# Optimization experiments

Measured on AMD Instinct MI355X. Metric: run time of the kernel, lower is better.

Reference implementation:

```python
import jax, jax.numpy as jnp
import numpy as np

B, N, D_IN, D, H, L, NQ, NC, HID = 4, 25000, 32, 256, 8, 6, 100, 18, 1024


def _ln(x, g, b, eps=1e-5):
    m = jnp.mean(x, -1, keepdims=True)
    v = jnp.mean((x - m) ** 2, -1, keepdims=True)
    return (x - m) / jnp.sqrt(v + eps) * g + b


def _mha(q, kv, wqkv, bqkv, wo, bo, h):
    # q: (B, Lq, d), kv: (B, Lk, d); torch nn.MultiheadAttention math
    d = q.shape[-1]
    dh = d // h
    wq, wk, wv = jnp.split(wqkv, 3, axis=0)
    bq, bk, bv = jnp.split(bqkv, 3)
    Q = (q @ wq.T + bq).reshape(q.shape[0], q.shape[1], h, dh)
    K = (kv @ wk.T + bk).reshape(kv.shape[0], kv.shape[1], h, dh)
    V = (kv @ wv.T + bv).reshape(kv.shape[0], kv.shape[1], h, dh)
    s = jnp.einsum('bqhd,bkhd->bhqk', Q, K) / jnp.asarray(np.sqrt(dh), Q.dtype)
    a = jax.nn.softmax(s, axis=-1)
    o = jnp.einsum('bhqk,bkhd->bqhd', a, V).reshape(q.shape)
    return o @ wo.T + bo


def setup_inputs() -> dict:
    key = jax.random.key(0)
    ks = list(jax.random.split(key, 20))
    ki = iter(ks)

    def p(shape, s=0.02):
        return jax.random.normal(next(ki), shape, jnp.float32) * s

    inp = {
        'x': jax.random.normal(next(ki), (B * N, D_IN), jnp.float32),
        'batch_offsets': jnp.arange(B + 1, dtype=jnp.int32) * N,
        'ip_w': p((D, D_IN)), 'ip_b': jnp.zeros((D,), jnp.float32),
        'ip_ln_g': jnp.ones((D,), jnp.float32), 'ip_ln_b': jnp.zeros((D,), jnp.float32),
        'xm_w1': p((D, D_IN)), 'xm_b1': jnp.zeros((D,), jnp.float32),
        'xm_w2': p((D, D)), 'xm_b2': jnp.zeros((D,), jnp.float32),
        'query_embed': p((NQ, D), 1.0),
        'ca_wqkv': p((L, 3 * D, D)), 'ca_bqkv': jnp.zeros((L, 3 * D), jnp.float32),
        'ca_wo': p((L, D, D)), 'ca_bo': jnp.zeros((L, D), jnp.float32),
        'sa_wqkv': p((L, 3 * D, D)), 'sa_bqkv': jnp.zeros((L, 3 * D), jnp.float32),
        'sa_wo': p((L, D, D)), 'sa_bo': jnp.zeros((L, D), jnp.float32),
        'sa_ln_g': jnp.ones((L, D), jnp.float32), 'sa_ln_b': jnp.zeros((L, D), jnp.float32),
        'ffn_w1': p((L, HID, D)), 'ffn_b1': jnp.zeros((L, HID), jnp.float32),
        'ffn_w2': p((L, D, HID)), 'ffn_b2': jnp.zeros((L, D), jnp.float32),
        'ffn_ln_g': jnp.ones((L, D), jnp.float32), 'ffn_ln_b': jnp.zeros((L, D), jnp.float32),
        'out_ln_g': jnp.ones((D,), jnp.float32), 'out_ln_b': jnp.zeros((D,), jnp.float32),
        'cls_w1': p((D, D)), 'cls_b1': jnp.zeros((D,), jnp.float32),
        'cls_w2': p((NC + 1, D)), 'cls_b2': jnp.zeros((NC + 1,), jnp.float32),
    }
    return inp


def reference(x, batch_offsets, ip_w, ip_b, ip_ln_g, ip_ln_b, xm_w1, xm_b1, xm_w2, xm_b2,
              query_embed, ca_wqkv, ca_bqkv, ca_wo, ca_bo, sa_wqkv, sa_bqkv, sa_wo, sa_bo,
              sa_ln_g, sa_ln_b, ffn_w1, ffn_b1, ffn_w2, ffn_b2, ffn_ln_g, ffn_ln_b,
              out_ln_g, out_ln_b, cls_w1, cls_b1, cls_w2, cls_b2):
    b = batch_offsets.shape[0] - 1  # uniform segments -> batched attention
    n = x.shape[0] // b
    # input_proj: Linear -> LayerNorm -> ReLU
    inst = jax.nn.relu(_ln(x @ ip_w.T + ip_b, ip_ln_g, ip_ln_b)).reshape(b, n, -1)
    # x_mask: Linear -> ReLU -> Linear
    mask_feats = (jax.nn.relu(x @ xm_w1.T + xm_b1) @ xm_w2.T + xm_b2).reshape(b, n, -1)
    query = jnp.broadcast_to(query_embed, (b,) + query_embed.shape)
    for i in range(ca_wqkv.shape[0]):
        # CrossAttentionLayer: NOTE original discards dropout/norm results -> pure residual
        query = _mha(query, inst, ca_wqkv[i], ca_bqkv[i], ca_wo[i], ca_bo[i], H) + query
        # SelfAttentionLayer: residual + LayerNorm
        query = _ln(_mha(query, query, sa_wqkv[i], sa_bqkv[i], sa_wo[i], sa_bo[i], H) + query,
                    sa_ln_g[i], sa_ln_b[i])
        # FFN: residual + LayerNorm
        ff = jax.nn.relu(query @ ffn_w1[i].T + ffn_b1[i]) @ ffn_w2[i].T + ffn_b2[i]
        query = _ln(ff + query, ffn_ln_g[i], ffn_ln_b[i])
    qn = _ln(query, out_ln_g, out_ln_b)
    pred_labels = jax.nn.relu(qn @ cls_w1.T + cls_b1) @ cls_w2.T + cls_b2  # (b, NQ, NC+1)
    pred_masks = jnp.einsum('bqd,bnd->bqn', qn, mask_feats)  # (b, NQ, n)
    return pred_labels, pred_masks
```

## Files before the change

kernel.cpp:

```cpp
#include <hip/hip_runtime.h>

typedef unsigned short u16;
typedef unsigned int   u32;

constexpr int Bz   = 4;
constexpr int Ni   = 25000;
constexpr int BNi  = Bz * Ni;
constexpr int DIN  = 32;
constexpr int D    = 256;
constexpr int Hh   = 8;
constexpr int DH   = 32;
constexpr int Ll   = 6;
constexpr int NQ   = 100;
constexpr int NC1  = 19;
constexpr int HIDd = 1024;

constexpr int CHUNK  = 1250;
constexpr int NCHUNK = Ni / CHUNK;
constexpr size_t PARTB = (size_t)Hh * NCHUNK * 128 * 34;
constexpr float SM_SCALE = 0.17677669529663687f;

__device__ __forceinline__ u16 f2b(float f) {
    union { __bf16 h; u16 u; } c; c.h = (__bf16)f; return c.u;
}
__device__ __forceinline__ u32 pk2(float a, float b) {
    union { __bf16 h[2]; u32 u; } c; c.h[0] = (__bf16)a; c.h[1] = (__bf16)b; return c.u;
}

__global__ void k_cvt(const float* __restrict__ in, u16* __restrict__ out, int n) {
    for (int i = blockIdx.x * blockDim.x + threadIdx.x; i < n; i += gridDim.x * blockDim.x)
        out[i] = f2b(in[i]);
}

struct CvtJobs { const float* s[9]; u16* d[9]; int n[9]; };
__global__ __launch_bounds__(256) void k_cvtall(CvtJobs j) {
    const int job = blockIdx.y;
    const float* s = j.s[job];
    u16* d = j.d[job];
    const int n = j.n[job];
    for (int i = blockIdx.x * 256 + threadIdx.x; i < n; i += gridDim.x * 256)
        d[i] = f2b(s[i]);
}

__device__ __forceinline__ void gload16(const u16* g, u16* l) {
    __builtin_amdgcn_global_load_lds(
        (const __attribute__((address_space(1))) void*)g,
        (__attribute__((address_space(3))) void*)l, 16, 0, 0);
}

typedef __attribute__((ext_vector_type(8))) __bf16 bf8v;
typedef __attribute__((ext_vector_type(8))) short  s8v;
typedef __attribute__((ext_vector_type(4))) float  f4v;

template<bool DOLN>
__global__ __launch_bounds__(512) void k_inproj(
    const float* __restrict__ x, int row0, int Mloc,
    const u16* __restrict__ w16, const float* __restrict__ bias,
    const float* __restrict__ g, const float* __restrict__ bb,
    u16* __restrict__ outb)
{
    __shared__ u16 Ws[256 * 40];
    __shared__ float Cb[256], Cg[256], Cbb[256];
    const int tid = threadIdx.x, lane = tid & 63, w = tid >> 6;
    const int lr = lane & 15, hi = lane >> 4;

    for (int ch = tid; ch < 1024; ch += 512) {
        int r = ch >> 2, g4 = ch & 3;
        *(uint4*)&Ws[r * 40 + g4 * 8] = *(const uint4*)(w16 + r * 32 + g4 * 8);
    }
    if (tid < 256) {
        Cb[tid] = bias[tid];
        if (DOLN) { Cg[tid] = g[tid]; Cbb[tid] = bb[tid]; }
    }

    const int rloc = blockIdx.x * 128 + w * 16 + lr;
    const int gr = row0 + min(rloc, Mloc - 1);
    bf8v xf;
    {
        const float* xp = x + (size_t)gr * DIN + hi * 8;
        float4 a = *(const float4*)xp, c = *(const float4*)(xp + 4);
        union { s8v s; bf8v b; } u;
        u.s[0] = (short)f2b(a.x); u.s[1] = (short)f2b(a.y);
        u.s[2] = (short)f2b(a.z); u.s[3] = (short)f2b(a.w);
        u.s[4] = (short)f2b(c.x); u.s[5] = (short)f2b(c.y);
        u.s[6] = (short)f2b(c.z); u.s[7] = (short)f2b(c.w);
        xf = u.b;
    }
    __syncthreads();

    f4v acc[16];
    #pragma unroll
    for (int ci = 0; ci < 16; ci++) {
        acc[ci] = (f4v){0.f, 0.f, 0.f, 0.f};
        bf8v af = *(const bf8v*)&Ws[(ci * 16 + lr) * 40 + hi * 8];
        acc[ci] = __builtin_amdgcn_mfma_f32_16x16x32_bf16(af, xf, acc[ci], 0, 0, 0);
    }
    #pragma unroll
    for (int ci = 0; ci < 16; ci++)
        #pragma unroll
        for (int r = 0; r < 4; r++)
            acc[ci][r] += Cb[ci * 16 + hi * 4 + r];

    float mean = 0.f, ri = 1.f;
    if (DOLN) {
        float s = 0.f, q = 0.f;
        #pragma unroll
        for (int ci = 0; ci < 16; ci++)
            #pragma unroll
            for (int r = 0; r < 4; r++) { s += acc[ci][r]; q += acc[ci][r] * acc[ci][r]; }
        s += __shfl_xor(s, 16); s += __shfl_xor(s, 32);
        q += __shfl_xor(q, 16); q += __shfl_xor(q, 32);
        mean = s * (1.f / D);
        float var = q * (1.f / D) - mean * mean;
        ri = rsqrtf(var + 1e-5f);
    }
    if (rloc < Mloc) {
        #pragma unroll
        for (int ci = 0; ci < 16; ci++) {
            float v0[4];
            #pragma unroll
            for (int r = 0; r < 4; r++) {
                float v = acc[ci][r];
                if (DOLN) v = (v - mean) * ri * Cg[ci * 16 + hi * 4 + r] + Cbb[ci * 16 + hi * 4 + r];
                v0[r] = fmaxf(v, 0.f);
            }
            uint2 pkv;
            pkv.x = pk2(v0[0], v0[1]);
            pkv.y = pk2(v0[2], v0[3]);
            *(uint2*)&outb[(size_t)rloc * 256 + ci * 16 + hi * 4] = pkv;
        }
    }
}

__global__ __launch_bounds__(256) void k_ln(
    const float* __restrict__ in, float* __restrict__ out,
    const float* __restrict__ g, const float* __restrict__ b)
{
    const int t = threadIdx.x;
    const int row = blockIdx.x;
    float v = in[(size_t)row * D + t];
    float s = v, q = v * v;
    #pragma unroll
    for (int off = 32; off >= 1; off >>= 1) { s += __shfl_xor(s, off); q += __shfl_xor(q, off); }
    __shared__ float red[2][4];
    const int wid = t >> 6;
    if ((t & 63) == 0) { red[0][wid] = s; red[1][wid] = q; }
    __syncthreads();
    float S = red[0][0] + red[0][1] + red[0][2] + red[0][3];
    float Q = red[1][0] + red[1][1] + red[1][2] + red[1][3];
    float m   = S * (1.f / D);
    float var = Q * (1.f / D) - m * m;
    float ri  = rsqrtf(var + 1e-5f);
    out[(size_t)row * D + t] = (v - m) * ri * g[t] + b[t];
}

__global__ __launch_bounds__(256) void k_bcast(const float* __restrict__ qe, float* __restrict__ q)
{
    const int t = threadIdx.x;
    const int r = blockIdx.x;
    q[(size_t)r * D + t] = qe[(size_t)(r % NQ) * D + t];
}

template<int BM, int BN, int TM, int TN>
__global__ __launch_bounds__(256) void k_gemm(
    const float* __restrict__ A, const float* __restrict__ W,
    const float* __restrict__ bias, const float* __restrict__ resid,
    float* __restrict__ C, int M, int N, int K, int relu)
{
    constexpr int BK = 16;
    constexpr int TX = BN / TN, TY = BM / TM;
    static_assert(TX * TY == 256, "block must be 256 threads");
    __shared__ float As[BK][BM + 4];
    __shared__ float Ws[BK][BN + 4];

    const int tid = threadIdx.x;
    const int tx = tid % TX, ty = tid / TX;
    const int row0 = blockIdx.y * BM, col0 = blockIdx.x * BN;

    float acc[TM][TN];
    #pragma unroll
    for (int i = 0; i < TM; i++)
        #pragma unroll
        for (int j = 0; j < TN; j++) acc[i][j] = 0.f;

    for (int k0 = 0; k0 < K; k0 += BK) {
        __syncthreads();
        for (int idx = tid; idx < BM * (BK / 4); idx += 256) {
            int r = idx / (BK / 4), c4 = idx % (BK / 4);
            int gr = row0 + r;
            float4 v;
            if (gr < M) v = *(const float4*)(A + (size_t)gr * K + k0 + c4 * 4);
            else { v.x = v.y = v.z = v.w = 0.f; }
            As[c4*4+0][r] = v.x; As[c4*4+1][r] = v.y; As[c4*4+2][r] = v.z; As[c4*4+3][r] = v.w;
        }
        for (int idx = tid; idx < BN * (BK / 4); idx += 256) {
            int n = idx / (BK / 4), c4 = idx % (BK / 4);
            int gn = col0 + n;
            float4 v;
            if (gn < N) v = *(const float4*)(W + (size_t)gn * K + k0 + c4 * 4);
            else { v.x = v.y = v.z = v.w = 0.f; }
            Ws[c4*4+0][n] = v.x; Ws[c4*4+1][n] = v.y; Ws[c4*4+2][n] = v.z; Ws[c4*4+3][n] = v.w;
        }
        __syncthreads();
        #pragma unroll
        for (int kk = 0; kk < BK; kk++) {
            float a[TM], bb[TN];
            #pragma unroll
            for (int i = 0; i < TM; i++) a[i] = As[kk][ty * TM + i];
            #pragma unroll
            for (int j = 0; j < TN; j++) bb[j] = Ws[kk][tx * TN + j];
            #pragma unroll
            for (int i = 0; i < TM; i++)
                #pragma unroll
                for (int j = 0; j < TN; j++)
                    acc[i][j] = fmaf(a[i], bb[j], acc[i][j]);
        }
    }

    #pragma unroll
    for (int i = 0; i < TM; i++) {
        int gr = row0 + ty * TM + i;
        if (gr >= M) continue;
        #pragma unroll
        for (int j = 0; j < TN; j++) {
            int gn = col0 + tx * TN + j;
            if (gn >= N) continue;
            float v = acc[i][j];
            if (bias)  v += bias[gn];
            if (resid) v += resid[(size_t)gr * N + gn];
            if (relu)  v = fmaxf(v, 0.f);
            C[(size_t)gr * N + gn] = v;
        }
    }
}

template<bool RELU>
__global__ __launch_bounds__(256) void mm_small(
    const float* __restrict__ A, const u16* __restrict__ W,
    const float* __restrict__ bias, const float* __restrict__ resid,
    float* __restrict__ C, int M, int N, int K)
{
    __shared__ u16 As[64 * 40];
    __shared__ u16 Bs[64 * 40];
    const int tid  = threadIdx.x;
    const int lane = tid & 63, w = tid >> 6;
    const int wm = w >> 1, wn = w & 1;
    const int row0 = blockIdx.y * 64, col0 = blockIdx.x * 64;
    const int lr = lane & 15, hi = lane >> 4;

    f4v acc[2][2];
    #pragma unroll
    for (int i = 0; i < 2; i++)
        #pragma unroll
        for (int j = 0; j < 2; j++) acc[i][j] = (f4v){0.f, 0.f, 0.f, 0.f};

    const int sr = tid >> 2, sc = (tid & 3) * 8;
    const float* ap = A + (size_t)min(row0 + sr, M - 1) * K + sc;
    const u16*   wpp = W + (size_t)min(col0 + sr, N - 1) * K + sc;
    u16* lA = &As[sr * 40 + sc];
    u16* lB = &Bs[sr * 40 + sc];

    for (int k0 = 0; k0 < K; k0 += 32) {
        __syncthreads();
        {
            float4 a = *(const float4*)ap, c = *(const float4*)(ap + 4);
            uint4 u;
            u.x = pk2(a.x, a.y); u.y = pk2(a.z, a.w);
            u.z = pk2(c.x, c.y); u.w = pk2(c.z, c.w);
            *(uint4*)lA = u;
            *(uint4*)lB = *(const uint4*)wpp;
            ap += 32; wpp += 32;
        }
        __syncthreads();
        bf8v a0 = *(const bf8v*)&As[(wm * 32      + lr) * 40 + hi * 8];
        bf8v a1 = *(const bf8v*)&As[(wm * 32 + 16 + lr) * 40 + hi * 8];
        bf8v b0 = *(const bf8v*)&Bs[(wn * 32      + lr) * 40 + hi * 8];
        bf8v b1 = *(const bf8v*)&Bs[(wn * 32 + 16 + lr) * 40 + hi * 8];
        acc[0][0] = __builtin_amdgcn_mfma_f32_16x16x32_bf16(a0, b0, acc[0][0], 0, 0, 0);
        acc[0][1] = __builtin_amdgcn_mfma_f32_16x16x32_bf16(a0, b1, acc[0][1], 0, 0, 0);
        acc[1][0] = __builtin_amdgcn_mfma_f32_16x16x32_bf16(a1, b0, acc[1][0], 0, 0, 0);
        acc[1][1] = __builtin_amdgcn_mfma_f32_16x16x32_bf16(a1, b1, acc[1][1], 0, 0, 0);
    }

    const int crl = hi * 4, ccl = lr;
    #pragma unroll
    for (int mi = 0; mi < 2; mi++)
        #pragma unroll
        for (int ni = 0; ni < 2; ni++)
            #pragma unroll
            for (int r = 0; r < 4; r++) {
                int grow = row0 + wm * 32 + mi * 16 + crl + r;
                int gcol = col0 + wn * 32 + ni * 16 + ccl;
                if (grow < M && gcol < N) {
                    float v = acc[mi][ni][r];
                    if (bias)  v += bias[gcol];
                    if (resid) v += resid[(size_t)grow * N + gcol];
                    if (RELU)  v = fmaxf(v, 0.f);
                    C[(size_t)grow * N + gcol] = v;
                }
            }
}

template<bool OUTBF>
__global__ __launch_bounds__(256) void mm128(
    const u16* __restrict__ A, const u16* __restrict__ W,
    const float* __restrict__ bias, void* __restrict__ Cv,
    int M, int N, int K, long long sA, long long sW, long long sC,
    int zmod, long long sW2, long long sBias)
{
    __shared__ u16 sm[8192];
    u16* As = sm;
    u16* Bs = sm + 4096;

    const int gx = gridDim.x, gy = gridDim.y;
    const int total = gx * gy * (int)gridDim.z;
    const int flat = blockIdx.x + gx * (blockIdx.y + gy * blockIdx.z);
    const int q8 = total >> 3, r8 = total & 7;
    const int xcd = flat & 7, blk = flat >> 3;
    const int swz = (xcd < r8 ? xcd * (q8 + 1) : r8 * (q8 + 1) + (xcd - r8) * q8) + blk;
    const int bx = swz % gx, by = (swz / gx) % gy, bz = swz / (gx * gy);

    const int aidx = bz % zmod, widx = bz / zmod;
    A += (size_t)aidx * sA;
    W += (size_t)aidx * sW + (size_t)widx * sW2;
    if (bias) bias += (size_t)widx * sBias;
    const int tid = threadIdx.x, lane = tid & 63, w = tid >> 6;
    const int wm = w >> 1, wn = w & 1;
    const int row0 = by * 128, col0 = bx * 128;
    const int lr = lane & 15, hi = lane >> 4;
    const int srow = lane >> 2, scol = (lane & 3) * 8;

    f4v acc[4][4];
    #pragma unroll
    for (int i = 0; i < 4; i++)
        #pragma unroll
        for (int j = 0; j < 4; j++) acc[i][j] = (f4v){0.f, 0.f, 0.f, 0.f};

    const int c0 = w * 2, c1 = w * 2 + 1;
    const u16* pa0 = A + (size_t)min(row0 + c0 * 16 + srow, M - 1) * K + scol;
    const u16* pa1 = A + (size_t)min(row0 + c1 * 16 + srow, M - 1) * K + scol;
    const u16* pb0 = W + (size_t)min(col0 + c0 * 16 + srow, N - 1) * K + scol;
    const u16* pb1 = W + (size_t)min(col0 + c1 * 16 + srow, N - 1) * K + scol;
    u16* la0 = &As[c0 * 512];
    u16* la1 = &As[c1 * 512];
    u16* lb0 = &Bs[c0 * 512];
    u16* lb1 = &Bs[c1 * 512];

    for (int k0 = 0; k0 < K; k0 += 32) {
        __syncthreads();
        gload16(pa0, la0); gload16(pa1, la1);
        gload16(pb0, lb0); gload16(pb1, lb1);
        pa0 += 32; pa1 += 32; pb0 += 32; pb1 += 32;
        __syncthreads();
        bf8v a[4], bb[4];
        #pragma unroll
        for (int mi = 0; mi < 4; mi++)
            a[mi] = *(const bf8v*)&As[(wm * 64 + mi * 16 + lr) * 32 + hi * 8];
        #pragma unroll
        for (int ni = 0; ni < 4; ni++)
            bb[ni] = *(const bf8v*)&Bs[(wn * 64 + ni * 16 + lr) * 32 + hi * 8];
        #pragma unroll
        for (int mi = 0; mi < 4; mi++)
            #pragma unroll
            for (int ni = 0; ni < 4; ni++)
                acc[mi][ni] = __builtin_amdgcn_mfma_f32_16x16x32_bf16(a[mi], bb[ni], acc[mi][ni], 0, 0, 0);
    }

    if (OUTBF) {
        #pragma unroll
        for (int h0 = 0; h0 < 2; h0++) {
            __syncthreads();
            if (wm == h0) {
                #pragma unroll
                for (int mi = 0; mi < 4; mi++)
                    #pragma unroll
                    for (int ni = 0; ni < 4; ni++) {
                        int gcol = col0 + wn * 64 + ni * 16 + lr;
                        float bv = bias ? bias[gcol] : 0.f;
                        #pragma unroll
                        for (int r = 0; r < 4; r++) {
                            int lrow = mi * 16 + hi * 4 + r;
                            sm[lrow * 128 + wn * 64 + ni * 16 + lr] = f2b(acc[mi][ni][r] + bv);
                        }
                    }
            }
            __syncthreads();
            u16* Cb16 = (u16*)Cv + (size_t)bz * sC;
            #pragma unroll
            for (int j = 0; j < 4; j++) {
                int idx = tid + j * 256;
                int lrow = idx >> 4, c16 = idx & 15;
                int grow = row0 + h0 * 64 + lrow;
                if (grow < M)
                    *(uint4*)(Cb16 + (size_t)grow * N + col0 + c16 * 8) =
                        *(const uint4*)&sm[lrow * 128 + c16 * 8];
            }
        }
    } else {
        const int crl = hi * 4, ccl = lr;
        float* Cf = (float*)Cv + (size_t)bz * sC;
        #pragma unroll
        for (int mi = 0; mi < 4; mi++)
            #pragma unroll
            for (int ni = 0; ni < 4; ni++)
                #pragma unroll
                for (int r = 0; r < 4; r++) {
                    int grow = row0 + wm * 64 + mi * 16 + crl + r;
                    int gcol = col0 + wn * 64 + ni * 16 + ccl;
                    if (grow < M && gcol < N) {
                        float v = acc[mi][ni][r];
                        if (bias) v += bias[gcol];
                        Cf[(size_t)grow * N + gcol] = v;
                    }
                }
    }
}

__global__ __launch_bounds__(512) void k_flash(
    const float* __restrict__ qbuf, const u16* __restrict__ kv,
    float* __restrict__ part, int bBase, size_t kvStride, size_t pStride)
{
    const int tid = threadIdx.x;
    const int lane = tid & 63, w = tid >> 6;
    const int h = blockIdx.y;
    const int b = bBase + blockIdx.z;
    const u16* kvp = kv + (size_t)blockIdx.z * kvStride;
    float* pp = part + (size_t)blockIdx.z * pStride;
    const int k0loc = blockIdx.x * CHUNK;
    const int lr = lane & 15, hi = lane >> 4;

    __shared__ u16 Ks[64 * 40];
    __shared__ u16 Vt[32 * 72];
    __shared__ u16 Pt[8][16 * 72];

    const int qt = w * 16 + lr;
    const int qg = b * NQ + min(qt, NQ - 1);
    bf8v qf;
    {
        const float* Qp = qbuf + (size_t)qg * D + h * DH + hi * 8;
        union { s8v s; bf8v b; } qu;
        #pragma unroll
        for (int j = 0; j < 8; j++) qu.s[j] = (short)f2b(Qp[j] * SM_SCALE);
        qf = qu.b;
    }

    const int keyK = (tid < 256) ? (tid >> 2) : ((tid - 256) >> 2);
    const int gK = (tid < 256) ? (tid & 3) : ((tid - 256) & 3);
    const u16* kvbase = kvp + h * DH + gK * 8 + (tid < 256 ? 0 : D);

    float m = -1e30f, l = 0.f;
    f4v o0 = (f4v){0.f,0.f,0.f,0.f}, o1 = (f4v){0.f,0.f,0.f,0.f};

    constexpr int NSTEP = (CHUNK + 63) / 64;
    for (int s = 0; s < NSTEP; s++) {
        const int ck = k0loc + s * 64;
        const int nv = min(64, k0loc + CHUNK - ck);
        __syncthreads();
        {
            int krow = min(ck + keyK, Ni - 1);
            if (tid < 256) {
                *(uint4*)&Ks[keyK * 40 + gK * 8] =
                    *(const uint4*)(kvbase + (size_t)krow * (2 * D));
            } else {
                uint4 u = *(const uint4*)(kvbase + (size_t)krow * (2 * D));
                const u16* pu = (const u16*)&u;
                #pragma unroll
                for (int j = 0; j < 8; j++) Vt[(gK * 8 + j) * 72 + keyK] = pu[j];
            }
        }
        __syncthreads();

        f4v sf[4];
        #pragma unroll
        for (int j = 0; j < 4; j++) {
            bf8v kf = *(const bf8v*)&Ks[(j * 16 + lr) * 40 + hi * 8];
            sf[j] = (f4v){0.f,0.f,0.f,0.f};
            sf[j] = __builtin_amdgcn_mfma_f32_16x16x32_bf16(kf, qf, sf[j], 0, 0, 0);
        }

        float sv[16];
        #pragma unroll
        for (int j = 0; j < 4; j++)
            #pragma unroll
            for (int r = 0; r < 4; r++) {
                int key0 = j * 16 + hi * 4 + r;
                sv[j * 4 + r] = (key0 < nv) ? sf[j][r] : -1e30f;
            }
        float smax = sv[0];
        #pragma unroll
        for (int j = 1; j < 16; j++) smax = fmaxf(smax, sv[j]);
        smax = fmaxf(smax, __shfl_xor(smax, 16));
        smax = fmaxf(smax, __shfl_xor(smax, 32));
        float mnew  = fmaxf(m, smax);
        float scale = __expf(m - mnew);
        m = mnew;

        float pv[16];
        float psum = 0.f;
        #pragma unroll
        for (int j = 0; j < 16; j++) {
            pv[j] = __expf(sv[j] - mnew);
            psum += pv[j];
        }
        psum += __shfl_xor(psum, 16);
        psum += __shfl_xor(psum, 32);
        l = l * scale + psum;

        u16* pw = &Pt[w][lr * 72];
        #pragma unroll
        for (int j = 0; j < 4; j++) {
            *(u32*)&pw[j * 16 + hi * 4]     = pk2(pv[j*4+0], pv[j*4+1]);
            *(u32*)&pw[j * 16 + hi * 4 + 2] = pk2(pv[j*4+2], pv[j*4+3]);
        }

        const int qb4 = hi * 4;
        float f0 = __shfl(scale, qb4 + 0);
        float f1 = __shfl(scale, qb4 + 1);
        float f2 = __shfl(scale, qb4 + 2);
        float f3 = __shfl(scale, qb4 + 3);
        o0[0] *= f0; o0[1] *= f1; o0[2] *= f2; o0[3] *= f3;
        o1[0] *= f0; o1[1] *= f1; o1[2] *= f2; o1[3] *= f3;

        #pragma unroll
        for (int j = 0; j < 2; j++) {
            bf8v pf  = *(const bf8v*)&Pt[w][lr * 72 + j * 32 + hi * 8];
            bf8v vf0 = *(const bf8v*)&Vt[lr * 72 + j * 32 + hi * 8];
            bf8v vf1 = *(const bf8v*)&Vt[(16 + lr) * 72 + j * 32 + hi * 8];
            o0 = __builtin_amdgcn_mfma_f32_16x16x32_bf16(pf, vf0, o0, 0, 0, 0);
            o1 = __builtin_amdgcn_mfma_f32_16x16x32_bf16(pf, vf1, o1, 0, 0, 0);
        }
    }

    const size_t pbase = ((size_t)(h * NCHUNK + blockIdx.x) * 128) * 34;
    #pragma unroll
    for (int r = 0; r < 4; r++) {
        int qtr = w * 16 + hi * 4 + r;
        pp[pbase + (size_t)qtr * 34 + 2 + lr]      = o0[r];
        pp[pbase + (size_t)qtr * 34 + 2 + 16 + lr] = o1[r];
    }
    if (lane < 16) {
        pp[pbase + (size_t)(w * 16 + lane) * 34 + 0] = m;
        pp[pbase + (size_t)(w * 16 + lane) * 34 + 1] = l;
    }
}

__global__ __launch_bounds__(64) void k_fmerge(const float* __restrict__ part,
                                               float* __restrict__ abuf, int bBase, size_t pStride)
{
    const float* pz = part + (size_t)blockIdx.y * pStride;
    const int b = bBase + blockIdx.y;
    const int t = threadIdx.x;
    const int hq = blockIdx.x;
    const int h = hq / NQ, q = hq % NQ;
    float mmax = -1e30f;
    for (int c = 0; c < NCHUNK; c++)
        mmax = fmaxf(mmax, pz[((size_t)(h * NCHUNK + c) * 128 + q) * 34]);
    float L = 0.f, a = 0.f;
    for (int c = 0; c < NCHUNK; c++) {
        const float* p = &pz[((size_t)(h * NCHUNK + c) * 128 + q) * 34];
        float wv = __expf(p[0] - mmax);
        L += wv * p[1];
        if (t < DH) a += wv * p[2 + t];
    }
    if (t < DH)
        abuf[((size_t)(b * NQ + q)) * D + h * DH + t] = a / L;
}

__global__ __launch_bounds__(128) void k_sattn(const float* __restrict__ sqkv, float* __restrict__ abuf)
{
    const int tid = threadIdx.x;
    const int bh = blockIdx.x;
    const int b = bh >> 3, h = bh & 7;
    __shared__ float Ks[NQ][DH], Vs[NQ][DH];
    for (int idx = tid; idx < NQ * 8; idx += 128) {
        int kk = idx >> 3, f4 = idx & 7;
        const float* base = sqkv + ((size_t)(b * NQ + kk)) * (3 * D) + h * DH;
        *(float4*)&Ks[kk][f4 * 4] = *(const float4*)(base + D + f4 * 4);
        *(float4*)&Vs[kk][f4 * 4] = *(const float4*)(base + 2 * D + f4 * 4);
    }
    float qr[DH];
    const int q = tid;
    if (q < NQ) {
        const float* Qp = sqkv + ((size_t)(b * NQ + q)) * (3 * D) + h * DH;
        #pragma unroll
        for (int d = 0; d < DH; d += 4) {
            float4 v = *(const float4*)(Qp + d);
            qr[d] = v.x * SM_SCALE; qr[d+1] = v.y * SM_SCALE;
            qr[d+2] = v.z * SM_SCALE; qr[d+3] = v.w * SM_SCALE;
        }
    } else {
        #pragma unroll
        for (int d = 0; d < DH; d++) qr[d] = 0.f;
    }
    __syncthreads();
    float m = -1e30f, l = 0.f, acc[DH];
    #pragma unroll
    for (int d = 0; d < DH; d++) acc[d] = 0.f;
    for (int kk = 0; kk < NQ; kk++) {
        float sc = 0.f;
        #pragma unroll
        for (int d = 0; d < DH; d++) sc += qr[d] * Ks[kk][d];
        if (sc > m) {
            float r = __expf(m - sc);
            l *= r;
            #pragma unroll
            for (int d = 0; d < DH; d++) acc[d] *= r;
            m = sc;
        }
        float p = __expf(sc - m);
        l += p;
        #pragma unroll
        for (int d = 0; d < DH; d++) acc[d] += p * Vs[kk][d];
    }
    if (q < NQ) {
        float li = 1.f / l;
        float* o = abuf + ((size_t)(b * NQ + q)) * D + h * DH;
        #pragma unroll
        for (int d = 0; d < DH; d++) o[d] = acc[d] * li;
    }
}

extern "C" void kernel_launch(void* const* d_in, const int* in_sizes, int n_in,
                              void* d_out, int out_size, void* d_ws, size_t ws_size,
                              hipStream_t stream)
{
    const float* x        = (const float*)d_in[0];
    const float* ip_w     = (const float*)d_in[2];
    const float* ip_b     = (const float*)d_in[3];
    const float* ip_g     = (const float*)d_in[4];
    const float* ip_bb    = (const float*)d_in[5];
    const float* xm_w1    = (const float*)d_in[6];
    const float* xm_b1    = (const float*)d_in[7];
    const float* xm_w2    = (const float*)d_in[8];
    const float* xm_b2    = (const float*)d_in[9];
    const float* qe       = (const float*)d_in[10];
    const float* ca_wqkv  = (const float*)d_in[11];
    const float* ca_bqkv  = (const float*)d_in[12];
    const float* ca_wo    = (const float*)d_in[13];
    const float* ca_bo    = (const float*)d_in[14];
    const float* sa_wqkv  = (const float*)d_in[15];
    const float* sa_bqkv  = (const float*)d_in[16];
    const float* sa_wo    = (const float*)d_in[17];
    const float* sa_bo    = (const float*)d_in[18];
    const float* sa_ln_g  = (const float*)d_in[19];
    const float* sa_ln_b  = (const float*)d_in[20];
    const float* ffn_w1   = (const float*)d_in[21];
    const float* ffn_b1   = (const float*)d_in[22];
    const float* ffn_w2   = (const float*)d_in[23];
    const float* ffn_b2   = (const float*)d_in[24];
    const float* ffn_ln_g = (const float*)d_in[25];
    const float* ffn_ln_b = (const float*)d_in[26];
    const float* out_ln_g = (const float*)d_in[27];
    const float* out_ln_b = (const float*)d_in[28];
    const float* cls_w1   = (const float*)d_in[29];
    const float* cls_b1   = (const float*)d_in[30];
    const float* cls_w2   = (const float*)d_in[31];
    const float* cls_b2   = (const float*)d_in[32];
    float* out = (float*)d_out;

    bool batched = false;
    int kvG = 1;
    int instRows;
    if      (ws_size >= 740000000ull) { batched = true; kvG = 6; instRows = BNi; }
    else if (ws_size >= 430000000ull) { batched = true; kvG = 3; instRows = BNi; }
    else if (ws_size >= 210000000ull) { batched = true; kvG = 1; instRows = BNi; }
    else if (ws_size >= 112000000ull) { instRows = BNi; }
    else if (ws_size >=  73000000ull) { instRows = Ni;  }
    else return;
    const bool instFull = (instRows == BNi);
    const int nzb = batched ? Bz : 1;

    char* wp = (char*)d_ws;
    auto alloc = [&](size_t bytes) -> char* {
        char* r = wp; wp += (bytes + 255) & ~(size_t)255; return r;
    };
    u16*   instb = (u16*)  alloc((size_t)instRows * D * 2);
    u16*   kvb   = (u16*)  alloc((batched ? (size_t)kvG * Bz * Ni * 2 * D : (size_t)Ni * 2 * D) * 2);
    float* part  = (float*)alloc((size_t)nzb * PARTB * 4);
    float* qbuf  = (float*)alloc(409600);
    float* abuf  = (float*)alloc(409600);
    float* sqkv  = (float*)alloc(1228800);
    float* f1b   = (float*)alloc(1638400);
    float* qA    = (float*)alloc(409600);
    float* qB    = (float*)alloc(409600);
    u16*   ipw16 = (u16*)  alloc(256 * 32 * 2);
    u16*   xw116 = (u16*)  alloc(256 * 32 * 2);
    u16*   xw216 = (u16*)  alloc((size_t)D * D * 2);
    u16*   caq16 = (u16*)  alloc((size_t)Ll * 3 * D * D * 2);
    u16*   saq16 = (u16*)  alloc((size_t)Ll * 3 * D * D * 2);
    u16*   cao16 = (u16*)  alloc((size_t)Ll * D * D * 2);
    u16*   sao16 = (u16*)  alloc((size_t)Ll * D * D * 2);
    u16*   fw116 = (u16*)  alloc((size_t)Ll * HIDd * D * 2);
    u16*   fw216 = (u16*)  alloc((size_t)Ll * D * HIDd * 2);
    u16*   qnb   = (u16*)  alloc((size_t)Bz * NQ * D * 2);

    {
        CvtJobs j;
        j.s[0] = ip_w;    j.d[0] = ipw16; j.n[0] = 256 * 32;
        j.s[1] = xm_w1;   j.d[1] = xw116; j.n[1] = 256 * 32;
        j.s[2] = xm_w2;   j.d[2] = xw216; j.n[2] = D * D;
        j.s[3] = ca_wqkv; j.d[3] = caq16; j.n[3] = Ll * 3 * D * D;
        j.s[4] = sa_wqkv; j.d[4] = saq16; j.n[4] = Ll * 3 * D * D;
        j.s[5] = ca_wo;   j.d[5] = cao16; j.n[5] = Ll * D * D;
        j.s[6] = sa_wo;   j.d[6] = sao16; j.n[6] = Ll * D * D;
        j.s[7] = ffn_w1;  j.d[7] = fw116; j.n[7] = Ll * HIDd * D;
        j.s[8] = ffn_w2;  j.d[8] = fw216; j.n[8] = Ll * D * HIDd;
        k_cvtall<<<dim3(48, 9), 256, 0, stream>>>(j);
    }

    if (instFull)
        k_inproj<true><<<(BNi + 127) / 128, 512, 0, stream>>>(
            x, 0, BNi, ipw16, ip_b, ip_g, ip_bb, instb);
    k_bcast<<<Bz * NQ, 256, 0, stream>>>(qe, qA);

    float* qcur = qA;
    float* qtmp = qB;

    auto layer_tail = [&](int i) {
        mm_small<false><<<dim3(4, 7), 256, 0, stream>>>(
            abuf, cao16 + (size_t)i * D * D, ca_bo + (size_t)i * D, qcur, qtmp,
            Bz * NQ, D, D);
        { float* t2 = qcur; qcur = qtmp; qtmp = t2; }
        mm_small<false><<<dim3(12, 7), 256, 0, stream>>>(
            qcur, saq16 + (size_t)i * 3 * D * D, sa_bqkv + (size_t)i * 3 * D, nullptr, sqkv,
            Bz * NQ, 3 * D, D);
        k_sattn<<<Bz * Hh, 128, 0, stream>>>(sqkv, abuf);
        mm_small<false><<<dim3(4, 7), 256, 0, stream>>>(
            abuf, sao16 + (size_t)i * D * D, sa_bo + (size_t)i * D, qcur, qtmp,
            Bz * NQ, D, D);
        k_ln<<<Bz * NQ, 256, 0, stream>>>(qtmp, qtmp, sa_ln_g + i * D, sa_ln_b + i * D);
        { float* t2 = qcur; qcur = qtmp; qtmp = t2; }
        mm_small<true><<<dim3(16, 7), 256, 0, stream>>>(
            qcur, fw116 + (size_t)i * HIDd * D, ffn_b1 + (size_t)i * HIDd, nullptr, f1b,
            Bz * NQ, HIDd, D);
        mm_small<false><<<dim3(4, 7), 256, 0, stream>>>(
            f1b, fw216 + (size_t)i * D * HIDd, ffn_b2 + (size_t)i * D, qcur, qtmp,
            Bz * NQ, D, HIDd);
        k_ln<<<Bz * NQ, 256, 0, stream>>>(qtmp, qtmp, ffn_ln_g + i * D, ffn_ln_b + i * D);
        { float* t2 = qcur; qcur = qtmp; qtmp = t2; }
    };

    if (batched) {
        for (int l0 = 0; l0 < Ll; l0 += kvG) {
            mm128<true><<<dim3(4, 196, 4 * kvG), 256, 0, stream>>>(
                instb, caq16 + (size_t)l0 * 3 * D * D + (size_t)D * D,
                ca_bqkv + (size_t)l0 * 3 * D + D, kvb, Ni, 2 * D, D,
                (long long)Ni * D, 0, (long long)Ni * 2 * D,
                4, (long long)3 * D * D, (long long)3 * D);
            for (int i = l0; i < l0 + kvG; i++) {
                const u16* wq16 = caq16 + (size_t)i * 3 * D * D;
                const float* bqkv = ca_bqkv + (size_t)i * 3 * D;
                mm_small<false><<<dim3(4, 7), 256, 0, stream>>>(
                    qcur, wq16, bqkv, nullptr, qbuf, Bz * NQ, D, D);
                const u16* kvl = kvb + (size_t)(i - l0) * Bz * Ni * 2 * D;
                k_flash<<<dim3(NCHUNK, Hh, 4), 512, 0, stream>>>(
                    qbuf, kvl, part, 0, (size_t)Ni * 2 * D, PARTB);
                k_fmerge<<<dim3(Hh * NQ, 4), 64, 0, stream>>>(part, abuf, 0, PARTB);
                layer_tail(i);
            }
        }
    } else {
        for (int i = 0; i < Ll; i++) {
            const u16* wq16  = caq16 + (size_t)i * 3 * D * D;
            const u16* wkv16 = wq16 + (size_t)D * D;
            const float* bqkv = ca_bqkv + (size_t)i * 3 * D;
            mm_small<false><<<dim3(4, 7), 256, 0, stream>>>(
                qcur, wq16, bqkv, nullptr, qbuf, Bz * NQ, D, D);
            for (int b = 0; b < Bz; b++) {
                if (!instFull)
                    k_inproj<true><<<(Ni + 127) / 128, 512, 0, stream>>>(
                        x, b * Ni, Ni, ipw16, ip_b, ip_g, ip_bb, instb);
                const u16* ip = instFull ? instb + (size_t)b * Ni * D : instb;
                mm128<true><<<dim3(4, 196, 1), 256, 0, stream>>>(
                    ip, wkv16, bqkv + D, kvb, Ni, 2 * D, D, 0, 0, 0, 4, 0, 0);
                k_flash<<<dim3(NCHUNK, Hh, 1), 512, 0, stream>>>(
                    qbuf, kvb, part, b, 0, 0);
                k_fmerge<<<dim3(Hh * NQ, 1), 64, 0, stream>>>(part, abuf, b, 0);
            }
            layer_tail(i);
        }
    }

    float* qn = qbuf;
    k_ln<<<Bz * NQ, 256, 0, stream>>>(qcur, qn, out_ln_g, out_ln_b);
    k_gemm<64,64,4,4><<<dim3(4, 7), 256, 0, stream>>>(
        qn, cls_w1, cls_b1, nullptr, abuf, Bz * NQ, D, D, 1);
    k_gemm<64,64,4,4><<<dim3(1, 7), 256, 0, stream>>>(
        abuf, cls_w2, cls_b2, nullptr, out, Bz * NQ, NC1, D, 0);

    k_cvt<<<128, 256, 0, stream>>>(qn, qnb, Bz * NQ * D);
    if (instFull) {
        k_inproj<false><<<(BNi + 127) / 128, 512, 0, stream>>>(
            x, 0, BNi, xw116, xm_b1, nullptr, nullptr, instb);
        if (batched) {
            mm128<true><<<dim3(2, 196, 4), 256, 0, stream>>>(
                instb, xw216, xm_b2, kvb, Ni, D, D,
                (long long)Ni * D, 0, (long long)Ni * D, 4, 0, 0);
            mm128<false><<<dim3(196, 1, 4), 256, 0, stream>>>(
                qnb, kvb, nullptr, out + Bz * NQ * NC1, NQ, Ni, D,
                (long long)NQ * D, (long long)Ni * D, (long long)NQ * Ni, 4, 0, 0);
        } else {
            for (int b = 0; b < Bz; b++) {
                mm128<true><<<dim3(2, 196, 1), 256, 0, stream>>>(
                    instb + (size_t)b * Ni * D, xw216, xm_b2, kvb, Ni, D, D, 0, 0, 0, 4, 0, 0);
                mm128<false><<<dim3(196, 1, 1), 256, 0, stream>>>(
                    qnb + (size_t)b * NQ * D, kvb, nullptr,
                    out + Bz * NQ * NC1 + (size_t)b * NQ * Ni, NQ, Ni, D, 0, 0, 0, 4, 0, 0);
            }
        }
    } else {
        for (int b = 0; b < Bz; b++) {
            k_inproj<false><<<(Ni + 127) / 128, 512, 0, stream>>>(
                x, b * Ni, Ni, xw116, xm_b1, nullptr, nullptr, instb);
            mm128<true><<<dim3(2, 196, 1), 256, 0, stream>>>(
                instb, xw216, xm_b2, kvb, Ni, D, D, 0, 0, 0, 4, 0, 0);
            mm128<false><<<dim3(196, 1, 1), 256, 0, stream>>>(
                qnb + (size_t)b * NQ * D, kvb, nullptr,
                out + Bz * NQ * NC1 + (size_t)b * NQ * Ni, NQ, Ni, D, 0, 0, 0, 4, 0, 0);
        }
    }
}
```

Baseline: 1.728 ms.

## Fuse per-layer attention tail into one cooperative persistent kernel with grid syncs

Replaces the chain of small per-layer launches (output projection, self-attention QKV, self-attention, projection, layernorm, two FFN GEMMs, layernorm) with a single cooperative kernel of 112 blocks that runs each stage with grid-wide syncs between them. It also removes the workspace-size-dependent paths so only the batched KV path with one layer per projection remains. The aim is to cut launch overhead and idle gaps for these tiny 400-row GEMMs. In exchange the tiles are small, each GEMM uses single-buffered LDS, and grid.sync carries its own cost. KV is now projected per layer instead of grouped across layers.

```diff
diff --git a/kernel.cpp b/kernel.cpp
--- a/kernel.cpp
+++ b/kernel.cpp
@@ -1,4 +1,7 @@
 #include <hip/hip_runtime.h>
+#include <hip/hip_cooperative_groups.h>
+
+namespace cg = cooperative_groups;
 
 typedef unsigned short u16;
 typedef unsigned int   u32;
@@ -14,6 +17,7 @@
 constexpr int NQ   = 100;
 constexpr int NC1  = 19;
 constexpr int HIDd = 1024;
+constexpr int MROW = Bz * NQ;
 
 constexpr int CHUNK  = 1250;
 constexpr int NCHUNK = Ni / CHUNK;
@@ -299,6 +303,191 @@
                     C[(size_t)grow * N + gcol] = v;
                 }
             }
+}
+
+__device__ void dev_mm(const float* A, const u16* W, const float* bias,
+                       const float* resid, float* C, int M, int N, int K,
+                       bool relu, char* smemc, int bid, int nb)
+{
+    u16* As = (u16*)smemc;
+    u16* Bs = (u16*)(smemc + 5120);
+    const int tid = threadIdx.x, lane = tid & 63, w = tid >> 6;
+    const int wm = w >> 1, wn = w & 1;
+    const int lr = lane & 15, hi = lane >> 4;
+    const int ntx = N >> 6, nty = (M + 63) >> 6;
+    const int sr = tid >> 2, sc = (tid & 3) * 8;
+    u16* lA = &As[sr * 40 + sc];
+    u16* lB = &Bs[sr * 40 + sc];
+
+    for (int t = bid; t < ntx * nty; t += nb) {
+        const int row0 = (t / ntx) * 64, col0 = (t % ntx) * 64;
+        f4v acc[2][2];
+        #pragma unroll
+        for (int i = 0; i < 2; i++)
+            #pragma unroll
+            for (int j = 0; j < 2; j++) acc[i][j] = (f4v){0.f, 0.f, 0.f, 0.f};
+
+        const float* ap = A + (size_t)min(row0 + sr, M - 1) * K + sc;
+        const u16*  wpp = W + (size_t)min(col0 + sr, N - 1) * K + sc;
+
+        for (int k0 = 0; k0 < K; k0 += 32) {
+            __syncthreads();
+            {
+                float4 a = *(const float4*)ap, c = *(const float4*)(ap + 4);
+                uint4 u;
+                u.x = pk2(a.x, a.y); u.y = pk2(a.z, a.w);
+                u.z = pk2(c.x, c.y); u.w = pk2(c.z, c.w);
+                *(uint4*)lA = u;
+                *(uint4*)lB = *(const uint4*)wpp;
+                ap += 32; wpp += 32;
+            }
+            __syncthreads();
+            bf8v a0 = *(const bf8v*)&As[(wm * 32      + lr) * 40 + hi * 8];
+            bf8v a1 = *(const bf8v*)&As[(wm * 32 + 16 + lr) * 40 + hi * 8];
+            bf8v b0 = *(const bf8v*)&Bs[(wn * 32      + lr) * 40 + hi * 8];
+            bf8v b1 = *(const bf8v*)&Bs[(wn * 32 + 16 + lr) * 40 + hi * 8];
+            acc[0][0] = __builtin_amdgcn_mfma_f32_16x16x32_bf16(a0, b0, acc[0][0], 0, 0, 0);
+            acc[0][1] = __builtin_amdgcn_mfma_f32_16x16x32_bf16(a0, b1, acc[0][1], 0, 0, 0);
+            acc[1][0] = __builtin_amdgcn_mfma_f32_16x16x32_bf16(a1, b0, acc[1][0], 0, 0, 0);
+            acc[1][1] = __builtin_amdgcn_mfma_f32_16x16x32_bf16(a1, b1, acc[1][1], 0, 0, 0);
+        }
+
+        const int crl = hi * 4, ccl = lr;
+        #pragma unroll
+        for (int mi = 0; mi < 2; mi++)
+            #pragma unroll
+            for (int ni = 0; ni < 2; ni++)
+                #pragma unroll
+                for (int r = 0; r < 4; r++) {
+                    int grow = row0 + wm * 32 + mi * 16 + crl + r;
+                    int gcol = col0 + wn * 32 + ni * 16 + ccl;
+                    if (grow < M && gcol < N) {
+                        float v = acc[mi][ni][r];
+                        if (bias)  v += bias[gcol];
+                        if (resid) v += resid[(size_t)grow * N + gcol];
+                        if (relu)  v = fmaxf(v, 0.f);
+                        C[(size_t)grow * N + gcol] = v;
+                    }
+                }
+        __syncthreads();
+    }
+}
+
+__device__ void dev_ln_ip(float* x, const float* g, const float* b,
+                          float* red, int bid, int nb)
+{
+    const int t = threadIdx.x;
+    for (int row = bid; row < MROW; row += nb) {
+        __syncthreads();
+        float v = x[(size_t)row * D + t];
+        float s = v, q = v * v;
+        #pragma unroll
+        for (int off = 32; off >= 1; off >>= 1) { s += __shfl_xor(s, off); q += __shfl_xor(q, off); }
+        const int wid = t >> 6;
+        if ((t & 63) == 0) { red[wid] = s; red[4 + wid] = q; }
+        __syncthreads();
+        float S = red[0] + red[1] + red[2] + red[3];
+        float Q = red[4] + red[5] + red[6] + red[7];
+        float m   = S * (1.f / D);
+        float var = Q * (1.f / D) - m * m;
+        float ri  = rsqrtf(var + 1e-5f);
+        x[(size_t)row * D + t] = (v - m) * ri * g[t] + b[t];
+    }
+}
+
+__device__ void dev_sattn(const float* sqkv, float* abuf, char* smemc, int bid)
+{
+    float (*Ks)[DH] = (float(*)[DH])smemc;
+    float (*Vs)[DH] = (float(*)[DH])(smemc + 12800);
+    const int tid = threadIdx.x;
+    const int b = bid >> 3, h = bid & 7;
+    for (int idx = tid; idx < NQ * 8; idx += 256) {
+        int kk = idx >> 3, f4 = idx & 7;
+        const float* base = sqkv + ((size_t)(b * NQ + kk)) * (3 * D) + h * DH;
+        *(float4*)&Ks[kk][f4 * 4] = *(const float4*)(base + D + f4 * 4);
+        *(float4*)&Vs[kk][f4 * 4] = *(const float4*)(base + 2 * D + f4 * 4);
+    }
+    float qr[DH];
+    const int q = tid;
+    if (q < NQ) {
+        const float* Qp = sqkv + ((size_t)(b * NQ + q)) * (3 * D) + h * DH;
+        #pragma unroll
+        for (int d = 0; d < DH; d += 4) {
+            float4 v = *(const float4*)(Qp + d);
+            qr[d] = v.x * SM_SCALE; qr[d+1] = v.y * SM_SCALE;
+            qr[d+2] = v.z * SM_SCALE; qr[d+3] = v.w * SM_SCALE;
+        }
+    } else {
+        #pragma unroll
+        for (int d = 0; d < DH; d++) qr[d] = 0.f;
+    }
+    __syncthreads();
+    float m = -1e30f, l = 0.f, acc[DH];
+    #pragma unroll
+    for (int d = 0; d < DH; d++) acc[d] = 0.f;
+    for (int kk = 0; kk < NQ; kk++) {
+        float sc = 0.f;
+        #pragma unroll
+        for (int d = 0; d < DH; d++) sc += qr[d] * Ks[kk][d];
+        if (sc > m) {
+            float r = __expf(m - sc);
+            l *= r;
+            #pragma unroll
+            for (int d = 0; d < DH; d++) acc[d] *= r;
+            m = sc;
+        }
+        float p = __expf(sc - m);
+        l += p;
+        #pragma unroll
+        for (int d = 0; d < DH; d++) acc[d] += p * Vs[kk][d];
+    }
+    if (q < NQ) {
+        float li = 1.f / l;
+        float* o = abuf + ((size_t)(b * NQ + q)) * D + h * DH;
+        #pragma unroll
+        for (int d = 0; d < DH; d++) o[d] = acc[d] * li;
+    }
+    __syncthreads();
+}
+
+struct TailArgs {
+    float* abuf;
+    float* qcur;
+    float* qtmp;
+    float* qbuf2;
+    float* sqkv;
+    float* f1b;
+    const u16* cao;  const float* ca_bo;
+    const u16* saq;  const float* sa_bq;
+    const u16* sao;  const float* sa_bo;
+    const float* sa_g; const float* sa_b;
+    const u16* fw1;  const float* fb1;
+    const u16* fw2;  const float* fb2;
+    const float* ff_g; const float* ff_b;
+};
+
+__global__ __launch_bounds__(256) void k_tail(TailArgs a)
+{
+    __shared__ char smem[25600];
+    __shared__ float red[8];
+    cg::grid_group grid = cg::this_grid();
+    const int bid = blockIdx.x, nb = gridDim.x;
+
+    dev_mm(a.abuf, a.cao, a.ca_bo, a.qcur, a.qtmp, MROW, D, D, false, smem, bid, nb);
+    grid.sync();
+    dev_mm(a.qtmp, a.saq, a.sa_bq, nullptr, a.sqkv, MROW, 3 * D, D, false, smem, bid, nb);
+    grid.sync();
+    if (bid < Bz * Hh) dev_sattn(a.sqkv, a.abuf, smem, bid);
+    grid.sync();
+    dev_mm(a.abuf, a.sao, a.sa_bo, a.qtmp, a.qbuf2, MROW, D, D, false, smem, bid, nb);
+    grid.sync();
+    dev_ln_ip(a.qbuf2, a.sa_g, a.sa_b, red, bid, nb);
+    grid.sync();
+    dev_mm(a.qbuf2, a.fw1, a.fb1, nullptr, a.f1b, MROW, HIDd, D, true, smem, bid, nb);
+    grid.sync();
+    dev_mm(a.f1b, a.fw2, a.fb2, a.qbuf2, a.qcur, MROW, D, HIDd, false, smem, bid, nb);
+    grid.sync();
+    dev_ln_ip(a.qcur, a.ff_g, a.ff_b, red, bid, nb);
 }
 
 template<bool OUTBF>
@@ -564,60 +753,6 @@
     }
     if (t < DH)
         abuf[((size_t)(b * NQ + q)) * D + h * DH + t] = a / L;
-}
-
-__global__ __launch_bounds__(128) void k_sattn(const float* __restrict__ sqkv, float* __restrict__ abuf)
-{
-    const int tid = threadIdx.x;
-    const int bh = blockIdx.x;
-    const int b = bh >> 3, h = bh & 7;
-    __shared__ float Ks[NQ][DH], Vs[NQ][DH];
-    for (int idx = tid; idx < NQ * 8; idx += 128) {
-        int kk = idx >> 3, f4 = idx & 7;
-        const float* base = sqkv + ((size_t)(b * NQ + kk)) * (3 * D) + h * DH;
-        *(float4*)&Ks[kk][f4 * 4] = *(const float4*)(base + D + f4 * 4);
-        *(float4*)&Vs[kk][f4 * 4] = *(const float4*)(base + 2 * D + f4 * 4);
-    }
-    float qr[DH];
-    const int q = tid;
-    if (q < NQ) {
-        const float* Qp = sqkv + ((size_t)(b * NQ + q)) * (3 * D) + h * DH;
-        #pragma unroll
-        for (int d = 0; d < DH; d += 4) {
-            float4 v = *(const float4*)(Qp + d);
-            qr[d] = v.x * SM_SCALE; qr[d+1] = v.y * SM_SCALE;
-            qr[d+2] = v.z * SM_SCALE; qr[d+3] = v.w * SM_SCALE;
-        }
-    } else {
-        #pragma unroll
-        for (int d = 0; d < DH; d++) qr[d] = 0.f;
-    }
-    __syncthreads();
-    float m = -1e30f, l = 0.f, acc[DH];
-    #pragma unroll
-    for (int d = 0; d < DH; d++) acc[d] = 0.f;
-    for (int kk = 0; kk < NQ; kk++) {
-        float sc = 0.f;
-        #pragma unroll
-        for (int d = 0; d < DH; d++) sc += qr[d] * Ks[kk][d];
-        if (sc > m) {
-            float r = __expf(m - sc);
-            l *= r;
-            #pragma unroll
-            for (int d = 0; d < DH; d++) acc[d] *= r;
-            m = sc;
-        }
-        float p = __expf(sc - m);
-        l += p;
-        #pragma unroll
-        for (int d = 0; d < DH; d++) acc[d] += p * Vs[kk][d];
-    }
-    if (q < NQ) {
-        float li = 1.f / l;
-        float* o = abuf + ((size_t)(b * NQ + q)) * D + h * DH;
-        #pragma unroll
-        for (int d = 0; d < DH; d++) o[d] = acc[d] * li;
-    }
 }
 
 extern "C" void kernel_launch(void* const* d_in, const int* in_sizes, int n_in,
@@ -658,31 +793,22 @@
     const float* cls_b2   = (const float*)d_in[32];
     float* out = (float*)d_out;
 
-    bool batched = false;
-    int kvG = 1;
-    int instRows;
-    if      (ws_size >= 740000000ull) { batched = true; kvG = 6; instRows = BNi; }
-    else if (ws_size >= 430000000ull) { batched = true; kvG = 3; instRows = BNi; }
-    else if (ws_size >= 210000000ull) { batched = true; kvG = 1; instRows = BNi; }
-    else if (ws_size >= 112000000ull) { instRows = BNi; }
-    else if (ws_size >=  73000000ull) { instRows = Ni;  }
-    else return;
-    const bool instFull = (instRows == BNi);
-    const int nzb = batched ? Bz : 1;
+    if (ws_size < 210000000ull) return;
 
     char* wp = (char*)d_ws;
     auto alloc = [&](size_t bytes) -> char* {
         char* r = wp; wp += (bytes + 255) & ~(size_t)255; return r;
     };
-    u16*   instb = (u16*)  alloc((size_t)instRows * D * 2);
-    u16*   kvb   = (u16*)  alloc((batched ? (size_t)kvG * Bz * Ni * 2 * D : (size_t)Ni * 2 * D) * 2);
-    float* part  = (float*)alloc((size_t)nzb * PARTB * 4);
+    u16*   instb = (u16*)  alloc((size_t)BNi * D * 2);
+    u16*   kvb   = (u16*)  alloc((size_t)Bz * Ni * 2 * D * 2);
+    float* part  = (float*)alloc((size_t)Bz * PARTB * 4);
     float* qbuf  = (float*)alloc(409600);
     float* abuf  = (float*)alloc(409600);
     float* sqkv  = (float*)alloc(1228800);
     float* f1b   = (float*)alloc(1638400);
     float* qA    = (float*)alloc(409600);
     float* qB    = (float*)alloc(409600);
+    float* qC    = (float*)alloc(409600);
     u16*   ipw16 = (u16*)  alloc(256 * 32 * 2);
     u16*   xw116 = (u16*)  alloc(256 * 32 * 2);
     u16*   xw216 = (u16*)  alloc((size_t)D * D * 2);
@@ -708,115 +834,54 @@
         k_cvtall<<<dim3(48, 9), 256, 0, stream>>>(j);
     }
 
-    if (instFull)
-        k_inproj<true><<<(BNi + 127) / 128, 512, 0, stream>>>(
-            x, 0, BNi, ipw16, ip_b, ip_g, ip_bb, instb);
+    k_inproj<true><<<(BNi + 127) / 128, 512, 0, stream>>>(
+        x, 0, BNi, ipw16, ip_b, ip_g, ip_bb, instb);
     k_bcast<<<Bz * NQ, 256, 0, stream>>>(qe, qA);
 
     float* qcur = qA;
-    float* qtmp = qB;
-
-    auto layer_tail = [&](int i) {
+
+    for (int i = 0; i < Ll; i++) {
+        const u16*   wq16  = caq16 + (size_t)i * 3 * D * D;
+        const u16*   wkv16 = wq16 + (size_t)D * D;
+        const float* bqkv  = ca_bqkv + (size_t)i * 3 * D;
         mm_small<false><<<dim3(4, 7), 256, 0, stream>>>(
-            abuf, cao16 + (size_t)i * D * D, ca_bo + (size_t)i * D, qcur, qtmp,
-            Bz * NQ, D, D);
-        { float* t2 = qcur; qcur = qtmp; qtmp = t2; }
-        mm_small<false><<<dim3(12, 7), 256, 0, stream>>>(
-            qcur, saq16 + (size_t)i * 3 * D * D, sa_bqkv + (size_t)i * 3 * D, nullptr, sqkv,
-            Bz * NQ, 3 * D, D);
-        k_sattn<<<Bz * Hh, 128, 0, stream>>>(sqkv, abuf);
-        mm_small<false><<<dim3(4, 7), 256, 0, stream>>>(
-            abuf, sao16 + (size_t)i * D * D, sa_bo + (size_t)i * D, qcur, qtmp,
-            Bz * NQ, D, D);
-        k_ln<<<Bz * NQ, 256, 0, stream>>>(qtmp, qtmp, sa_ln_g + i * D, sa_ln_b + i * D);
-        { float* t2 = qcur; qcur = qtmp; qtmp = t2; }
-        mm_small<true><<<dim3(16, 7), 256, 0, stream>>>(
-            qcur, fw116 + (size_t)i * HIDd * D, ffn_b1 + (size_t)i * HIDd, nullptr, f1b,
-            Bz * NQ, HIDd, D);
-        mm_small<false><<<dim3(4, 7), 256, 0, stream>>>(
-            f1b, fw216 + (size_t)i * D * HIDd, ffn_b2 + (size_t)i * D, qcur, qtmp,
-            Bz * NQ, D, HIDd);
-        k_ln<<<Bz * NQ, 256, 0, stream>>>(qtmp, qtmp, ffn_ln_g + i * D, ffn_ln_b + i * D);
-        { float* t2 = qcur; qcur = qtmp; qtmp = t2; }
-    };
-
-    if (batched) {
-        for (int l0 = 0; l0 < Ll; l0 += kvG) {
-            mm128<true><<<dim3(4, 196, 4 * kvG), 256, 0, stream>>>(
-                instb, caq16 + (size_t)l0 * 3 * D * D + (size_t)D * D,
-                ca_bqkv + (size_t)l0 * 3 * D + D, kvb, Ni, 2 * D, D,
-                (long long)Ni * D, 0, (long long)Ni * 2 * D,
-                4, (long long)3 * D * D, (long long)3 * D);
-            for (int i = l0; i < l0 + kvG; i++) {
-                const u16* wq16 = caq16 + (size_t)i * 3 * D * D;
-                const float* bqkv = ca_bqkv + (size_t)i * 3 * D;
-                mm_small<false><<<dim3(4, 7), 256, 0, stream>>>(
-                    qcur, wq16, bqkv, nullptr, qbuf, Bz * NQ, D, D);
-                const u16* kvl = kvb + (size_t)(i - l0) * Bz * Ni * 2 * D;
-                k_flash<<<dim3(NCHUNK, Hh, 4), 512, 0, stream>>>(
-                    qbuf, kvl, part, 0, (size_t)Ni * 2 * D, PARTB);
-                k_fmerge<<<dim3(Hh * NQ, 4), 64, 0, stream>>>(part, abuf, 0, PARTB);
-                layer_tail(i);
-            }
-        }
-    } else {
-        for (int i = 0; i < Ll; i++) {
-            const u16* wq16  = caq16 + (size_t)i * 3 * D * D;
-            const u16* wkv16 = wq16 + (size_t)D * D;
-            const float* bqkv = ca_bqkv + (size_t)i * 3 * D;
-            mm_small<false><<<dim3(4, 7), 256, 0, stream>>>(
-                qcur, wq16, bqkv, nullptr, qbuf, Bz * NQ, D, D);
-            for (int b = 0; b < Bz; b++) {
-                if (!instFull)
-                    k_inproj<true><<<(Ni + 127) / 128, 512, 0, stream>>>(
-                        x, b * Ni, Ni, ipw16, ip_b, ip_g, ip_bb, instb);
-                const u16* ip = instFull ? instb + (size_t)b * Ni * D : instb;
-                mm128<true><<<dim3(4, 196, 1), 256, 0, stream>>>(
-                    ip, wkv16, bqkv + D, kvb, Ni, 2 * D, D, 0, 0, 0, 4, 0, 0);
-                k_flash<<<dim3(NCHUNK, Hh, 1), 512, 0, stream>>>(
-                    qbuf, kvb, part, b, 0, 0);
-                k_fmerge<<<dim3(Hh * NQ, 1), 64, 0, stream>>>(part, abuf, b, 0);
-            }
-            layer_tail(i);
-        }
+            qcur, wq16, bqkv, nullptr, qbuf, MROW, D, D);
+        mm128<true><<<dim3(4, 196, 4), 256, 0, stream>>>(
+            instb, wkv16, bqkv + D, kvb, Ni, 2 * D, D,
+            (long long)Ni * D, 0, (long long)Ni * 2 * D,
+            4, 0, 0);
+        k_flash<<<dim3(NCHUNK, Hh, 4), 512, 0, stream>>>(
+            qbuf, kvb, part, 0, (size_t)Ni * 2 * D, PARTB);
+        k_fmerge<<<dim3(Hh * NQ, 4), 64, 0, stream>>>(part, abuf, 0, PARTB);
+        TailArgs ta;
+        ta.abuf = abuf; ta.qcur = qcur; ta.qtmp = qB; ta.qbuf2 = qC;
+        ta.sqkv = sqkv; ta.f1b = f1b;
+        ta.cao = cao16 + (size_t)i * D * D;      ta.ca_bo = ca_bo + (size_t)i * D;
+        ta.saq = saq16 + (size_t)i * 3 * D * D;  ta.sa_bq = sa_bqkv + (size_t)i * 3 * D;
+        ta.sao = sao16 + (size_t)i * D * D;      ta.sa_bo = sa_bo + (size_t)i * D;
+        ta.sa_g = sa_ln_g + (size_t)i * D;       ta.sa_b = sa_ln_b + (size_t)i * D;
+        ta.fw1 = fw116 + (size_t)i * HIDd * D;   ta.fb1 = ffn_b1 + (size_t)i * HIDd;
+        ta.fw2 = fw216 + (size_t)i * D * HIDd;   ta.fb2 = ffn_b2 + (size_t)i * D;
+        ta.ff_g = ffn_ln_g + (size_t)i * D;      ta.ff_b = ffn_ln_b + (size_t)i * D;
+        void* kargs[] = { (void*)&ta };
+        hipLaunchCooperativeKernel((const void*)k_tail, dim3(112), dim3(256),
+                                   kargs, 0, stream);
     }
 
     float* qn = qbuf;
     k_ln<<<Bz * NQ, 256, 0, stream>>>(qcur, qn, out_ln_g, out_ln_b);
     k_gemm<64,64,4,4><<<dim3(4, 7), 256, 0, stream>>>(
-        qn, cls_w1, cls_b1, nullptr, abuf, Bz * NQ, D, D, 1);
+        qn, cls_w1, cls_b1, nullptr, abuf, MROW, D, D, 1);
     k_gemm<64,64,4,4><<<dim3(1, 7), 256, 0, stream>>>(
-        abuf, cls_w2, cls_b2, nullptr, out, Bz * NQ, NC1, D, 0);
+        abuf, cls_w2, cls_b2, nullptr, out, MROW, NC1, D, 0);
 
     k_cvt<<<128, 256, 0, stream>>>(qn, qnb, Bz * NQ * D);
-    if (instFull) {
-        k_inproj<false><<<(BNi + 127) / 128, 512, 0, stream>>>(
-            x, 0, BNi, xw116, xm_b1, nullptr, nullptr, instb);
-        if (batched) {
-            mm128<true><<<dim3(2, 196, 4), 256, 0, stream>>>(
-                instb, xw216, xm_b2, kvb, Ni, D, D,
-                (long long)Ni * D, 0, (long long)Ni * D, 4, 0, 0);
-            mm128<false><<<dim3(196, 1, 4), 256, 0, stream>>>(
-                qnb, kvb, nullptr, out + Bz * NQ * NC1, NQ, Ni, D,
-                (long long)NQ * D, (long long)Ni * D, (long long)NQ * Ni, 4, 0, 0);
-        } else {
-            for (int b = 0; b < Bz; b++) {
-                mm128<true><<<dim3(2, 196, 1), 256, 0, stream>>>(
-                    instb + (size_t)b * Ni * D, xw216, xm_b2, kvb, Ni, D, D, 0, 0, 0, 4, 0, 0);
-                mm128<false><<<dim3(196, 1, 1), 256, 0, stream>>>(
-                    qnb + (size_t)b * NQ * D, kvb, nullptr,
-                    out + Bz * NQ * NC1 + (size_t)b * NQ * Ni, NQ, Ni, D, 0, 0, 0, 4, 0, 0);
-            }
-        }
-    } else {
-        for (int b = 0; b < Bz; b++) {
-            k_inproj<false><<<(Ni + 127) / 128, 512, 0, stream>>>(
-                x, b * Ni, Ni, xw116, xm_b1, nullptr, nullptr, instb);
-            mm128<true><<<dim3(2, 196, 1), 256, 0, stream>>>(
-                instb, xw216, xm_b2, kvb, Ni, D, D, 0, 0, 0, 4, 0, 0);
-            mm128<false><<<dim3(196, 1, 1), 256, 0, stream>>>(
-                qnb + (size_t)b * NQ * D, kvb, nullptr,
-                out + Bz * NQ * NC1 + (size_t)b * NQ * Ni, NQ, Ni, D, 0, 0, 0, 4, 0, 0);
-        }
-    }
-}
+    k_inproj<false><<<(BNi + 127) / 128, 512, 0, stream>>>(
+        x, 0, BNi, xw116, xm_b1, nullptr, nullptr, instb);
+    mm128<true><<<dim3(2, 196, 4), 256, 0, stream>>>(
+        instb, xw216, xm_b2, kvb, Ni, D, D,
+        (long long)Ni * D, 0, (long long)Ni * D, 4, 0, 0);
+    mm128<false><<<dim3(196, 1, 4), 256, 0, stream>>>(
+        qnb, kvb, nullptr, out + Bz * NQ * NC1, NQ, Ni, D,
+        (long long)NQ * D, (long long)Ni * D, (long long)NQ * Ni, 4, 0, 0);
+}
```

New measurement: 2.259 ms. 1.31x slower.
